# Kernel optimization log

Hardware: AMD Instinct MI355X
Metric: run time of the kernel (lower is better)

Reference implementation:

```python
import jax, jax.numpy as jnp
import numpy as np

D_MODEL = 128
NEG_INF = -1e30


def setup_inputs() -> dict:
    key = jax.random.key(0)
    k1, k2, k3, k4 = jax.random.split(key, 4)
    B, Lc, Lq, d = 32, 2048, 256, D_MODEL
    C = jax.random.normal(k1, (B, Lc, d), dtype=jnp.float32)
    Q = jax.random.normal(k2, (B, Lq, d), dtype=jnp.float32)
    # Linear(3d, 1): weight laid out for cat order (Q_, C_, C_*Q_)
    w = jax.random.normal(k3, (3 * d,), dtype=jnp.float32) / np.sqrt(3 * d)
    b = jax.random.normal(k4, (1,), dtype=jnp.float32) * 0.01
    c_mask = jnp.ones((B, Lc), dtype=jnp.int32)
    q_mask = jnp.ones((B, Lq), dtype=jnp.int32)
    return {"C": C, "Q": Q, "w": w, "b": b, "c_mask": c_mask, "q_mask": q_mask}


def reference(C, Q, w, b, c_mask, q_mask):
    d = C.shape[-1]
    # Algebraic decomposition of Linear([Q_, C_, C_*Q_]) -> scalar:
    # S[b,i,j] = Q[b,j]@w_q + C[b,i]@w_c + (C[b,i]*w_m)@Q[b,j] + bias
    w_q, w_c, w_m = w[:d], w[d:2 * d], w[2 * d:]
    S = (C @ w_c)[:, :, None] \
        + (Q @ w_q)[:, None, :] \
        + jnp.einsum('bid,bjd->bij', C * w_m, Q) \
        + b[0]                                        # (B, Lc, Lq)
    mask = (c_mask[:, :, None] * q_mask[:, None, :]).astype(S.dtype)
    S = S * mask + NEG_INF * (1.0 - mask)
    S1 = jax.nn.softmax(S, axis=1)  # softmax over context dim (as in source)
    S2 = jax.nn.softmax(S, axis=2)  # softmax over query dim
    C2Q = jnp.einsum('bij,bjd->bid', S1, Q)           # (B, Lc, d)
    # Q2C = S1 @ S2^T @ C, associated as S1 @ (S2^T @ C) to avoid (Lc,Lc)
    T = jnp.einsum('bkj,bkd->bjd', S2, C)             # (B, Lq, d)
    Q2C = jnp.einsum('bij,bjd->bid', S1, T)           # (B, Lc, d)
    out = jnp.concatenate([C, C2Q, C * C2Q, C * Q2C], axis=2)  # (B, Lc, 4d)
    # dropout omitted (deterministic reference / eval mode)
    return out
```

## Files before the change

### kernel.cpp

```cpp
#include <hip/hip_runtime.h>


#define LC 2048
#define LQ 256
#define DM 128
#define NEG_INF_F (-1e30f)

using bf16x8  = __attribute__((ext_vector_type(8))) __bf16;
using f32x4   = __attribute__((ext_vector_type(4))) float;
using ushort8 = __attribute__((ext_vector_type(8))) unsigned short;

__device__ __forceinline__ unsigned short f2bf(float x) {
    unsigned int u = __float_as_uint(x);
    u += 0x7fffu + ((u >> 16) & 1u);
    return (unsigned short)(u >> 16);
}
__device__ __forceinline__ float bf2f(unsigned short h) {
    return __uint_as_float(((unsigned int)h) << 16);
}
__device__ __forceinline__ f32x4 mfma16(bf16x8 a, bf16x8 b, f32x4 c) {
    return __builtin_amdgcn_mfma_f32_16x16x32_bf16(a, b, c, 0, 0, 0);
}

__global__ __launch_bounds__(256) void k_preQ(const float* __restrict__ Q,
        const float* __restrict__ w, unsigned short* __restrict__ Qbf,
        unsigned short* __restrict__ Qt, float* __restrict__ rq) {
    const int b = blockIdx.z, j0 = blockIdx.x * 64, d0 = blockIdx.y * 64;
    const int tid = threadIdx.x;
    __shared__ float tile[64][65];
    __shared__ float wq[128];
    if (tid < 128) wq[tid] = w[tid];
    __syncthreads();
    const int r = tid >> 2, c0 = (tid & 3) * 16;
    const float4* sp = (const float4*)(Q + (size_t)(b * LQ + j0 + r) * DM + d0 + c0);
    float v[16];
#pragma unroll
    for (int u = 0; u < 4; ++u) {
        float4 t = sp[u];
        v[4*u] = t.x; v[4*u+1] = t.y; v[4*u+2] = t.z; v[4*u+3] = t.w;
    }
    unsigned short ob[16];
    float p = 0.f;
#pragma unroll
    for (int u = 0; u < 16; ++u) {
        ob[u] = f2bf(v[u]);
        p += v[u] * wq[d0 + c0 + u];
        tile[r][c0 + u] = v[u];
    }
    ushort8* qb = (ushort8*)(Qbf + (size_t)(b * LQ + j0 + r) * DM + d0 + c0);
    qb[0] = *(ushort8*)&ob[0];
    qb[1] = *(ushort8*)&ob[8];
    p += __shfl_xor(p, 1);
    p += __shfl_xor(p, 2);
    if ((tid & 3) == 0) atomicAdd(&rq[b * LQ + j0 + r], p);
    __syncthreads();
    unsigned short o[16];
#pragma unroll
    for (int u = 0; u < 16; ++u) o[u] = f2bf(tile[c0 + u][r]);
    ushort8* dp = (ushort8*)(Qt + (size_t)(b * DM + d0 + r) * LQ + j0 + c0);
    dp[0] = *(ushort8*)&o[0];
    dp[1] = *(ushort8*)&o[8];
}

__global__ __launch_bounds__(256) void k1_scores(
    const float* __restrict__ C, const unsigned short* __restrict__ Qbf,
    const float* __restrict__ w, const float* __restrict__ bptr,
    const int* __restrict__ c_mask, const int* __restrict__ q_mask,
    const float* __restrict__ rq,
    unsigned short* __restrict__ E, unsigned short* __restrict__ Ct,
    float* __restrict__ l1g, float* __restrict__ l2g) {
    const int b = blockIdx.y;
    const int i0 = blockIdx.x * 64;
    const int tid = threadIdx.x;
    const int lane = tid & 63, wid = tid >> 6;
    const int quad = lane >> 4, l15 = lane & 15;

    __shared__ unsigned short Alds[64][136];
    __shared__ float wsm[256];
    __shared__ float rcs[64], rqs[256], cms[64], qms[256], l2s[64];
    __shared__ float b0s;

    if (tid < 256) {
        wsm[tid] = w[128 + tid];
        rqs[tid] = rq[b * LQ + tid];
        qms[tid] = (float)q_mask[b * LQ + tid];
    }
    if (tid < 64) {
        cms[tid] = (float)c_mask[b * LC + i0 + tid];
        l2s[tid] = 0.f;
    }
    if (tid == 0) b0s = bptr[0];
    __syncthreads();

    {
        const int r = tid >> 2, qq = tid & 3;
        const float4* cp = (const float4*)(C + (size_t)(b * LC + i0 + r) * DM + qq * 32);
        unsigned short* ctb = Ct + (size_t)b * DM * LC + i0 + r;
        float prc = 0.f;
#pragma unroll
        for (int u = 0; u < 8; ++u) {
            float4 v = cp[u];
            const int c0 = qq * 32 + u * 4;
            prc += v.x * wsm[c0] + v.y * wsm[c0 + 1] + v.z * wsm[c0 + 2] + v.w * wsm[c0 + 3];
            Alds[r][c0 + 0] = f2bf(v.x * wsm[128 + c0]);
            Alds[r][c0 + 1] = f2bf(v.y * wsm[129 + c0]);
            Alds[r][c0 + 2] = f2bf(v.z * wsm[130 + c0]);
            Alds[r][c0 + 3] = f2bf(v.w * wsm[131 + c0]);
            ctb[(size_t)(c0 + 0) * LC] = f2bf(v.x);
            ctb[(size_t)(c0 + 1) * LC] = f2bf(v.y);
            ctb[(size_t)(c0 + 2) * LC] = f2bf(v.z);
            ctb[(size_t)(c0 + 3) * LC] = f2bf(v.w);
        }
        prc += __shfl_xor(prc, 1);
        prc += __shfl_xor(prc, 2);
        if (qq == 0) rcs[r] = prc;
    }
    __syncthreads();

    const int n_base = wid * 64;
    const unsigned short* qbase = Qbf + (size_t)b * LQ * DM;
    const f32x4 z4 = {0.f, 0.f, 0.f, 0.f};
    f32x4 acc[4][4];
#pragma unroll
    for (int mt = 0; mt < 4; ++mt)
#pragma unroll
        for (int nt = 0; nt < 4; ++nt) acc[mt][nt] = z4;

#pragma unroll
    for (int kc = 0; kc < 4; ++kc) {
        const int ko = kc * 32 + quad * 8;
        bf16x8 af[4], bfr[4];
#pragma unroll
        for (int mt = 0; mt < 4; ++mt)
            af[mt] = *(const bf16x8*)&Alds[mt * 16 + l15][ko];
#pragma unroll
        for (int nt = 0; nt < 4; ++nt)
            bfr[nt] = *(const bf16x8*)(qbase + (size_t)(n_base + nt * 16 + l15) * DM + ko);
#pragma unroll
        for (int mt = 0; mt < 4; ++mt)
#pragma unroll
            for (int nt = 0; nt < 4; ++nt)
                acc[mt][nt] = mfma16(af[mt], bfr[nt], acc[mt][nt]);
    }

    const float b0 = b0s;
    float colsum[4] = {0.f, 0.f, 0.f, 0.f};
#pragma unroll
    for (int mt = 0; mt < 4; ++mt) {
#pragma unroll
        for (int reg = 0; reg < 4; ++reg) {
            const int m = mt * 16 + quad * 4 + reg;
            float rowsum = 0.f;
#pragma unroll
            for (int nt = 0; nt < 4; ++nt) {
                const int n = n_base + nt * 16 + l15;
                float s = acc[mt][nt][reg] + rcs[m] + rqs[n] + b0;
                const float mk = cms[m] * qms[n];
                s = s * mk + NEG_INF_F * (1.f - mk);
                const float e = __expf(s);
                acc[mt][nt][reg] = e;
                rowsum += e;
                colsum[nt] += e;
            }
            rowsum += __shfl_xor(rowsum, 1);
            rowsum += __shfl_xor(rowsum, 2);
            rowsum += __shfl_xor(rowsum, 4);
            rowsum += __shfl_xor(rowsum, 8);
            if (l15 == 0) atomicAdd(&l2s[m], rowsum);
        }
    }
#pragma unroll
    for (int nt = 0; nt < 4; ++nt) {
        float v = colsum[nt];
        v += __shfl_xor(v, 16);
        v += __shfl_xor(v, 32);
        if (quad == 0) atomicAdd(&l1g[b * LQ + n_base + nt * 16 + l15], v);
    }
    __syncthreads();
    if (tid < 64) l2g[b * LC + i0 + tid] = l2s[tid];

#pragma unroll
    for (int mt = 0; mt < 4; ++mt) {
#pragma unroll
        for (int reg = 0; reg < 4; ++reg) {
            const int m = mt * 16 + quad * 4 + reg;
            const float rl = 1.0f / l2s[m];
            unsigned short* erow = E + (size_t)(b * LC + i0 + m) * LQ;
#pragma unroll
            for (int nt = 0; nt < 4; ++nt) {
                const int n = n_base + nt * 16 + l15;
                erow[n] = f2bf(acc[mt][nt][reg] * rl);
            }
        }
    }
}

__global__ __launch_bounds__(512) void k3_Tt(
    const unsigned short* __restrict__ E, const unsigned short* __restrict__ Ct,
    const unsigned short* __restrict__ Qt, const float* __restrict__ l1g,
    unsigned short* __restrict__ Qts, unsigned short* __restrict__ Tt) {
    const int id = blockIdx.x;
    const int t = id >> 3;
    const int jt = t & 3, dt = (t >> 2) & 1;
    const int b = ((t >> 3) << 3) | (id & 7);
    const int j0 = jt * 64, d0 = dt * 64;
    const int tid = threadIdx.x;
    const int lane = tid & 63, wid = tid >> 6;
    const int quad = lane >> 4, l15 = lane & 15;
    const int m_base = (wid >> 1) * 16, n32 = (wid & 1) * 32;

    __shared__ unsigned short Ab[64][136];
    __shared__ unsigned short Bb[64][136];
    __shared__ float rl1s[64];
    if (tid < 64) rl1s[tid] = 1.0f / l1g[b * LQ + j0 + tid];
    __syncthreads();

    if (dt == 0) {
        const int r = tid >> 2, jq = (tid & 3) * 16;
        const ushort8* qp = (const ushort8*)(Qt + (size_t)(b * DM + r) * LQ + j0 + jq);
        ushort8 v0 = qp[0], v1 = qp[1];
        unsigned short o[16];
#pragma unroll
        for (int u = 0; u < 8; ++u) o[u] = f2bf(bf2f(v0[u]) * rl1s[jq + u]);
#pragma unroll
        for (int u = 0; u < 8; ++u) o[8 + u] = f2bf(bf2f(v1[u]) * rl1s[jq + 8 + u]);
        ushort8* op = (ushort8*)(Qts + (size_t)(b * DM + r) * LQ + j0 + jq);
        op[0] = *(ushort8*)&o[0];
        op[1] = *(ushort8*)&o[8];
    }

    const f32x4 z4 = {0.f, 0.f, 0.f, 0.f};
    f32x4 acc[2] = {z4, z4};

    for (int it = 0; it < 16; ++it) {
        const int ic = it * 128;
        __syncthreads();
        {
            const int r = tid >> 3, q = tid & 7;
            const ushort8* cp = (const ushort8*)(Ct + (size_t)(b * DM + d0 + r) * LC + ic + q * 16);
            *(ushort8*)&Ab[r][q * 16] = cp[0];
            *(ushort8*)&Ab[r][q * 16 + 8] = cp[1];
        }
        {
            const int il = tid >> 2, sg = (tid & 3) * 16;
            const ushort8* ep = (const ushort8*)(E + (size_t)(b * LC + ic + il) * LQ + j0 + sg);
            ushort8 e0 = ep[0], e1 = ep[1];
#pragma unroll
            for (int u = 0; u < 8; ++u) Bb[sg + u][il] = e0[u];
#pragma unroll
            for (int u = 0; u < 8; ++u) Bb[sg + 8 + u][il] = e1[u];
        }
        __syncthreads();
#pragma unroll
        for (int kk = 0; kk < 4; ++kk) {
            const int ko = kk * 32 + quad * 8;
            bf16x8 af = *(const bf16x8*)&Ab[m_base + l15][ko];
            bf16x8 b0f = *(const bf16x8*)&Bb[n32 + l15][ko];
            bf16x8 b1f = *(const bf16x8*)&Bb[n32 + 16 + l15][ko];
            acc[0] = mfma16(af, b0f, acc[0]);
            acc[1] = mfma16(af, b1f, acc[1]);
        }
    }
#pragma unroll
    for (int nt = 0; nt < 2; ++nt)
#pragma unroll
        for (int reg = 0; reg < 4; ++reg) {
            const int dd = d0 + m_base + quad * 4 + reg;
            const int jl = n32 + nt * 16 + l15;
            Tt[(size_t)(b * DM + dd) * LQ + j0 + jl] = f2bf(acc[nt][reg] * rl1s[jl]);
        }
}

__global__ __launch_bounds__(256) void k4_out(
    const unsigned short* __restrict__ E, const float* __restrict__ C,
    const unsigned short* __restrict__ Qts, const unsigned short* __restrict__ Tt,
    const float* __restrict__ l2g, float* __restrict__ out) {
    const int b = blockIdx.y;
    const int i0 = blockIdx.x * 64;
    const int tid = threadIdx.x;
    const int lane = tid & 63, wid = tid >> 6;
    const int quad = lane >> 4, l15 = lane & 15;
    const int n_base = wid * 32;

    __shared__ unsigned short Aq[64][72];
    __shared__ unsigned short Bq[128][72];
    __shared__ unsigned short Bt2[128][72];
    __shared__ float l2s[64];
    if (tid < 64) l2s[tid] = l2g[b * LC + i0 + tid];

    const f32x4 z4 = {0.f, 0.f, 0.f, 0.f};
    f32x4 acc1[4][2], acc2[4][2];
#pragma unroll
    for (int mt = 0; mt < 4; ++mt)
#pragma unroll
        for (int nt = 0; nt < 2; ++nt) { acc1[mt][nt] = z4; acc2[mt][nt] = z4; }

#pragma unroll 1
    for (int kc = 0; kc < 4; ++kc) {
        const int jc = kc * 64;
        __syncthreads();
        {
            const int r = tid >> 2, q = tid & 3;
            const ushort8* ep = (const ushort8*)(E + (size_t)(b * LC + i0 + r) * LQ + jc + q * 16);
            *(ushort8*)&Aq[r][q * 16] = ep[0];
            *(ushort8*)&Aq[r][q * 16 + 8] = ep[1];
        }
        {
            const int r = tid >> 1, h = (tid & 1) * 32;
            const ushort8* qp = (const ushort8*)(Qts + (size_t)(b * DM + r) * LQ + jc + h);
            const ushort8* tp = (const ushort8*)(Tt + (size_t)(b * DM + r) * LQ + jc + h);
#pragma unroll
            for (int u = 0; u < 4; ++u) {
                *(ushort8*)&Bq[r][h + u * 8] = qp[u];
                *(ushort8*)&Bt2[r][h + u * 8] = tp[u];
            }
        }
        __syncthreads();
#pragma unroll
        for (int kk = 0; kk < 2; ++kk) {
            const int ko = kk * 32 + quad * 8;
            bf16x8 a[4], bq[2], bt[2];
#pragma unroll
            for (int mt = 0; mt < 4; ++mt)
                a[mt] = *(const bf16x8*)&Aq[mt * 16 + l15][ko];
#pragma unroll
            for (int nt = 0; nt < 2; ++nt) {
                bq[nt] = *(const bf16x8*)&Bq[n_base + nt * 16 + l15][ko];
                bt[nt] = *(const bf16x8*)&Bt2[n_base + nt * 16 + l15][ko];
            }
#pragma unroll
            for (int mt = 0; mt < 4; ++mt)
#pragma unroll
                for (int nt = 0; nt < 2; ++nt) {
                    acc1[mt][nt] = mfma16(a[mt], bq[nt], acc1[mt][nt]);
                    acc2[mt][nt] = mfma16(a[mt], bt[nt], acc2[mt][nt]);
                }
        }
    }

#pragma unroll
    for (int mt = 0; mt < 4; ++mt)
#pragma unroll
        for (int reg = 0; reg < 4; ++reg) {
            const int il = mt * 16 + quad * 4 + reg;
            const int i = i0 + il;
            const float l2v = l2s[il];
            const size_t rb = (size_t)(b * LC + i) * 512;
            const float* crow = C + (size_t)(b * LC + i) * DM;
#pragma unroll
            for (int nt = 0; nt < 2; ++nt) {
                const int d = n_base + nt * 16 + l15;
                const float c = crow[d];
                const float v1 = acc1[mt][nt][reg] * l2v;
                const float v2 = acc2[mt][nt][reg] * l2v;
                out[rb + d] = c;
                out[rb + 128 + d] = v1;
                out[rb + 256 + d] = c * v1;
                out[rb + 384 + d] = c * v2;
            }
        }
}

extern "C" void kernel_launch(void* const* d_in, const int* in_sizes, int n_in,
                              void* d_out, int out_size, void* d_ws, size_t ws_size,
                              hipStream_t stream) {
    const float* C = (const float*)d_in[0];
    const float* Q = (const float*)d_in[1];
    const float* w = (const float*)d_in[2];
    const float* bp = (const float*)d_in[3];
    const int* cm = (const int*)d_in[4];
    const int* qm = (const int*)d_in[5];
    float* out = (float*)d_out;

    char* ws = (char*)d_ws;
    unsigned short* E   = (unsigned short*)(ws);
    unsigned short* Ct  = (unsigned short*)(ws + 33554432);
    unsigned short* Qbf = (unsigned short*)(ws + 50331648);
    unsigned short* Qt  = (unsigned short*)(ws + 52428800);
    unsigned short* Qts = (unsigned short*)(ws + 54525952);
    unsigned short* Tt  = (unsigned short*)(ws + 56623104);
    float*          l2g = (float*)(ws + 58720256);
    float*          rq  = (float*)(ws + 58982400);
    float*          l1  = (float*)(ws + 59015168);

    hipMemsetAsync(ws + 58982400, 0, 65536, stream);

    k_preQ<<<dim3(4, 2, 32), 256, 0, stream>>>(Q, w, Qbf, Qt, rq);
    k1_scores<<<dim3(32, 32), 256, 0, stream>>>(C, Qbf, w, bp, cm, qm, rq, E, Ct, l1, l2g);
    k3_Tt<<<dim3(256), 512, 0, stream>>>(E, Ct, Qt, l1, Qts, Tt);
    k4_out<<<dim3(32, 32), 256, 0, stream>>>(E, C, Qts, Tt, l2g, out);
}
```

Baseline: 241.0 us.

## Fold masks into score biases, load whole E tile once, read B operands from global

In k1_scores, the c/q masks and the bias are folded into the per-row and per-column bias arrays. A masked row or column becomes -inf, which removes the per-element mask multiply and blend. In k4_out, the full 64x256 E tile is staged into LDS once, and the Qts/Tt B-fragments are read straight from global (L2) instead of being staged through LDS with two barriers per chunk. The grid is flattened and remapped so neighbouring blocks share a batch's Qts/Tt in cache. The change cuts barriers and LDS traffic, but makes k4 more sensitive to global load latency and uses more LDS per block.

```diff
diff --git a/kernel.cpp b/kernel.cpp
--- a/kernel.cpp
+++ b/kernel.cpp
@@ -77,19 +77,14 @@
 
     __shared__ unsigned short Alds[64][136];
     __shared__ float wsm[256];
-    __shared__ float rcs[64], rqs[256], cms[64], qms[256], l2s[64];
-    __shared__ float b0s;
+    __shared__ float rcs[64], rqs[256], l2s[64];
 
     if (tid < 256) {
         wsm[tid] = w[128 + tid];
-        rqs[tid] = rq[b * LQ + tid];
-        qms[tid] = (float)q_mask[b * LQ + tid];
-    }
-    if (tid < 64) {
-        cms[tid] = (float)c_mask[b * LC + i0 + tid];
-        l2s[tid] = 0.f;
-    }
-    if (tid == 0) b0s = bptr[0];
+        const float qm = (float)q_mask[b * LQ + tid];
+        rqs[tid] = (qm != 0.f) ? (rq[b * LQ + tid] + bptr[0]) : NEG_INF_F;
+    }
+    if (tid < 64) l2s[tid] = 0.f;
     __syncthreads();
 
     {
@@ -113,7 +108,10 @@
         }
         prc += __shfl_xor(prc, 1);
         prc += __shfl_xor(prc, 2);
-        if (qq == 0) rcs[r] = prc;
+        if (qq == 0) {
+            const float cmv = (float)c_mask[b * LC + i0 + r];
+            rcs[r] = (cmv != 0.f) ? prc : NEG_INF_F;
+        }
     }
     __syncthreads();
 
@@ -143,7 +141,6 @@
                 acc[mt][nt] = mfma16(af[mt], bfr[nt], acc[mt][nt]);
     }
 
-    const float b0 = b0s;
     float colsum[4] = {0.f, 0.f, 0.f, 0.f};
 #pragma unroll
     for (int mt = 0; mt < 4; ++mt) {
@@ -154,9 +151,7 @@
 #pragma unroll
             for (int nt = 0; nt < 4; ++nt) {
                 const int n = n_base + nt * 16 + l15;
-                float s = acc[mt][nt][reg] + rcs[m] + rqs[n] + b0;
-                const float mk = cms[m] * qms[n];
-                s = s * mk + NEG_INF_F * (1.f - mk);
+                const float s = acc[mt][nt][reg] + rcs[m] + rqs[n];
                 const float e = __expf(s);
                 acc[mt][nt][reg] = e;
                 rowsum += e;
@@ -275,19 +270,28 @@
     const unsigned short* __restrict__ E, const float* __restrict__ C,
     const unsigned short* __restrict__ Qts, const unsigned short* __restrict__ Tt,
     const float* __restrict__ l2g, float* __restrict__ out) {
-    const int b = blockIdx.y;
-    const int i0 = blockIdx.x * 64;
+    const int id = blockIdx.x;
+    const int b = (id & 7) | ((id >> 8) << 3);
+    const int i0 = ((id >> 3) & 31) * 64;
     const int tid = threadIdx.x;
     const int lane = tid & 63, wid = tid >> 6;
     const int quad = lane >> 4, l15 = lane & 15;
     const int n_base = wid * 32;
 
-    __shared__ unsigned short Aq[64][72];
-    __shared__ unsigned short Bq[128][72];
-    __shared__ unsigned short Bt2[128][72];
+    __shared__ unsigned short Aq[64][264];
     __shared__ float l2s[64];
     if (tid < 64) l2s[tid] = l2g[b * LC + i0 + tid];
 
+    {
+        const int r = tid >> 2, c0 = (tid & 3) * 64;
+        const ushort8* ep = (const ushort8*)(E + (size_t)(b * LC + i0 + r) * LQ + c0);
+#pragma unroll
+        for (int u = 0; u < 8; ++u) *(ushort8*)&Aq[r][c0 + u * 8] = ep[u];
+    }
+    __syncthreads();
+
+    const unsigned short* qsb = Qts + (size_t)b * DM * LQ;
+    const unsigned short* ttb = Tt  + (size_t)b * DM * LQ;
     const f32x4 z4 = {0.f, 0.f, 0.f, 0.f};
     f32x4 acc1[4][2], acc2[4][2];
 #pragma unroll
@@ -295,47 +299,26 @@
 #pragma unroll
         for (int nt = 0; nt < 2; ++nt) { acc1[mt][nt] = z4; acc2[mt][nt] = z4; }
 
-#pragma unroll 1
-    for (int kc = 0; kc < 4; ++kc) {
-        const int jc = kc * 64;
-        __syncthreads();
-        {
-            const int r = tid >> 2, q = tid & 3;
-            const ushort8* ep = (const ushort8*)(E + (size_t)(b * LC + i0 + r) * LQ + jc + q * 16);
-            *(ushort8*)&Aq[r][q * 16] = ep[0];
-            *(ushort8*)&Aq[r][q * 16 + 8] = ep[1];
-        }
-        {
-            const int r = tid >> 1, h = (tid & 1) * 32;
-            const ushort8* qp = (const ushort8*)(Qts + (size_t)(b * DM + r) * LQ + jc + h);
-            const ushort8* tp = (const ushort8*)(Tt + (size_t)(b * DM + r) * LQ + jc + h);
-#pragma unroll
-            for (int u = 0; u < 4; ++u) {
-                *(ushort8*)&Bq[r][h + u * 8] = qp[u];
-                *(ushort8*)&Bt2[r][h + u * 8] = tp[u];
+#pragma unroll 2
+    for (int ks = 0; ks < 8; ++ks) {
+        const int ko = ks * 32 + quad * 8;
+        bf16x8 a[4], bq[2], bt[2];
+#pragma unroll
+        for (int mt = 0; mt < 4; ++mt)
+            a[mt] = *(const bf16x8*)&Aq[mt * 16 + l15][ko];
+#pragma unroll
+        for (int nt = 0; nt < 2; ++nt) {
+            const size_t roff = (size_t)(n_base + nt * 16 + l15) * LQ + ko;
+            bq[nt] = *(const bf16x8*)(qsb + roff);
+            bt[nt] = *(const bf16x8*)(ttb + roff);
+        }
+#pragma unroll
+        for (int mt = 0; mt < 4; ++mt)
+#pragma unroll
+            for (int nt = 0; nt < 2; ++nt) {
+                acc1[mt][nt] = mfma16(a[mt], bq[nt], acc1[mt][nt]);
+                acc2[mt][nt] = mfma16(a[mt], bt[nt], acc2[mt][nt]);
             }
-        }
-        __syncthreads();
-#pragma unroll
-        for (int kk = 0; kk < 2; ++kk) {
-            const int ko = kk * 32 + quad * 8;
-            bf16x8 a[4], bq[2], bt[2];
-#pragma unroll
-            for (int mt = 0; mt < 4; ++mt)
-                a[mt] = *(const bf16x8*)&Aq[mt * 16 + l15][ko];
-#pragma unroll
-            for (int nt = 0; nt < 2; ++nt) {
-                bq[nt] = *(const bf16x8*)&Bq[n_base + nt * 16 + l15][ko];
-                bt[nt] = *(const bf16x8*)&Bt2[n_base + nt * 16 + l15][ko];
-            }
-#pragma unroll
-            for (int mt = 0; mt < 4; ++mt)
-#pragma unroll
-                for (int nt = 0; nt < 2; ++nt) {
-                    acc1[mt][nt] = mfma16(a[mt], bq[nt], acc1[mt][nt]);
-                    acc2[mt][nt] = mfma16(a[mt], bt[nt], acc2[mt][nt]);
-                }
-        }
     }
 
 #pragma unroll
@@ -388,5 +371,5 @@
     k_preQ<<<dim3(4, 2, 32), 256, 0, stream>>>(Q, w, Qbf, Qt, rq);
     k1_scores<<<dim3(32, 32), 256, 0, stream>>>(C, Qbf, w, bp, cm, qm, rq, E, Ct, l1, l2g);
     k3_Tt<<<dim3(256), 512, 0, stream>>>(E, Ct, Qt, l1, Qts, Tt);
-    k4_out<<<dim3(32, 32), 256, 0, stream>>>(E, C, Qts, Tt, l2g, out);
-}
+    k4_out<<<dim3(1024), 256, 0, stream>>>(E, C, Qts, Tt, l2g, out);
+}
```

Measured after the change: 241.8 us. Within noise of the previous version (+0.3%).
